# Kernel tuning notes

Hardware: AMD Instinct MI355X
Metric: run time of the kernel (lower is better)

## Reference

```python
import jax, jax.numpy as jnp
import numpy as np

E = 300000          # number of edges
C_IN = 128          # in_channels (source/target feature dim)
C_E = 128           # edge_channels
C_OUT = 128         # out_channels (== in_channels, required by AttentionBlock residual)
C8 = C_OUT // 8     # attention bottleneck dim


def _lin(key, fan_in, fan_out):
    # torch nn.Linear default: U(-1/sqrt(fan_in), 1/sqrt(fan_in)) for W and b
    kw, kb = jax.random.split(key)
    bound = 1.0 / np.sqrt(fan_in)
    w = jax.random.uniform(kw, (fan_in, fan_out), jnp.float32, -bound, bound)
    b = jax.random.uniform(kb, (fan_out,), jnp.float32, -bound, bound)
    return w, b


def setup_inputs() -> dict:
    key = jax.random.key(0)
    ks = jax.random.split(key, 10)
    w1, b1 = _lin(ks[3], 2 * C_IN + C_E, C_OUT)   # edge_mlp[0]
    w2, b2 = _lin(ks[4], C_OUT, C_OUT)            # edge_mlp[2]
    wg, bg = _lin(ks[5], C_OUT, C8)               # att.g
    wt, bt = _lin(ks[6], C_OUT, C8)               # att.theta
    wp, bp = _lin(ks[7], C_OUT, C8)               # att.phi
    wo, bo = _lin(ks[8], C8, C_OUT)               # att.W
    return {
        "source": jax.random.normal(ks[0], (E, C_IN), jnp.float32),
        "target": jax.random.normal(ks[1], (E, C_IN), jnp.float32),
        "edge_attr": jax.random.normal(ks[2], (E, C_E), jnp.float32),
        "w1": w1, "b1": b1, "w2": w2, "b2": b2,
        "wg": wg, "bg": bg, "wt": wt, "bt": bt,
        "wp": wp, "bp": bp, "wo": wo, "bo": bo,
    }


def reference(source, target, edge_attr, w1, b1, w2, b2, wg, bg, wt, bt, wp, bp, wo, bo):
    # edge_mlp: Linear -> ReLU -> Linear on concat(source, target, edge_attr)
    x = jnp.concatenate([source, target, edge_attr], axis=1)        # [E, 2*C_IN + C_E]
    h = jax.nn.relu(x @ w1 + b1)                                    # [E, C_OUT]
    h = h @ w2 + b2                                                 # [E, C_OUT]
    # AttentionBlock (AtLoc-style): rank-1 outer-product attention over bottleneck dim
    g = h @ wg + bg                                                 # [E, C8]
    th = h @ wt + bt                                                # [E, C8]
    ph = h @ wp + bp                                                # [E, C8]
    f = ph[:, :, None] * th[:, None, :]                             # [E, C8, C8] = phi_x @ theta_x^T
    a = jax.nn.softmax(f, axis=-1)                                  # softmax over last dim
    y = jnp.einsum("eij,ej->ei", a, g)                              # [E, C8]
    return y @ wo + bo + h                                          # residual add, [E, C_OUT]
```

## Files before the change

### kernel.cpp

```cpp
#include <hip/hip_runtime.h>
#include <hip/hip_bf16.h>

typedef unsigned short u16;
typedef unsigned int u32;
typedef __bf16 bf16x8 __attribute__((ext_vector_type(8)));
typedef float f32x4 __attribute__((ext_vector_type(4)));

#define NE 300000
#define NBLK 2344

#define WS_WT1   0
#define WS_WT2   49152
#define WS_WGTP  65536
#define WS_WO    71680
#define WS_TOTAL 75776
#define WS_BF32  37888
#define NBIAS    432
#define WS_FLAG32 38320

__device__ __forceinline__ float bs2f(u16 u) {
    union { u32 i; float f; } v; v.i = ((u32)u) << 16; return v.f;
}
__device__ __forceinline__ u16 f2bs(float f) {
    __hip_bfloat16 h = __float2bfloat16(f);
    u16 u; __builtin_memcpy(&u, &h, 2); return u;
}
__device__ __forceinline__ __bf16 f2b(float f) {
    __hip_bfloat16 h = __float2bfloat16(f);
    __bf16 b; __builtin_memcpy(&b, &h, 2); return b;
}

#define LDFRAG(arr, row, kch) (*(const bf16x8*)&(arr)[(row) * 128 + ((((kch) ^ ((row) & 15))) << 3)])
#define SWZ(row, col) ((row) * 128 + (((((col) >> 3) ^ ((row) & 15))) << 3) + ((col) & 7))

__global__ void sniff_kernel(const void* __restrict__ src, u32* __restrict__ wsu) {
    if (threadIdx.x != 0) return;
    const u32* p = (const u32*)src;
    int score = 0;
    for (int i = 0; i < 64; ++i) {
        u32 w = p[i];
        int e = (w >> 7) & 0xFF;
        score += (e > 100 && e < 150) ? 1 : 0;
    }
    wsu[WS_FLAG32] = (score >= 40) ? 1u : 0u;
}

__global__ void prep_kernel(const void* __restrict__ w1, const void* __restrict__ w2,
                            const void* __restrict__ wg, const void* __restrict__ wt,
                            const void* __restrict__ wp, const void* __restrict__ wo,
                            const void* __restrict__ b1, const void* __restrict__ b2,
                            const void* __restrict__ bg, const void* __restrict__ bt,
                            const void* __restrict__ bp, const void* __restrict__ bo,
                            u16* __restrict__ ws) {
    const bool isbf = ((const u32*)ws)[WS_FLAG32] != 0;
    auto ldf = [&](const void* p, int idx) -> float {
        return isbf ? bs2f(((const u16*)p)[idx]) : ((const float*)p)[idx];
    };
    int id = blockIdx.x * 256 + threadIdx.x;
    if (id < WS_TOTAL) {
        float v;
        if (id < WS_WT2) {
            int c = id >> 14, r = id & 16383, n = r >> 7, k = r & 127;
            v = ldf(w1, (c * 128 + k) * 128 + n);
        } else if (id < WS_WGTP) {
            int r = id - WS_WT2, n = r >> 7, k = r & 127;
            v = ldf(w2, k * 128 + n);
        } else if (id < WS_WO) {
            int r = id - WS_WGTP, n = r >> 7, k = r & 127;
            if (n < 16)      v = ldf(wg, k * 16 + n);
            else if (n < 32) v = ldf(wt, k * 16 + (n - 16));
            else             v = ldf(wp, k * 16 + (n - 32));
        } else {
            int r = id - WS_WO, n = r >> 5, k = r & 31;
            v = (k < 16) ? ldf(wo, k * 128 + n) : 0.f;
        }
        ws[id] = f2bs(v);
    } else if (id < WS_TOTAL + NBIAS) {
        int b = id - WS_TOTAL;
        float v;
        if (b < 128)      v = ldf(b1, b);
        else if (b < 256) v = ldf(b2, b - 128);
        else if (b < 272) v = ldf(bg, b - 256);
        else if (b < 288) v = ldf(bt, b - 272);
        else if (b < 304) v = ldf(bp, b - 288);
        else              v = ldf(bo, b - 304);
        ((float*)ws)[WS_BF32 + b] = v;
    }
}

#define GEMM_K128(NACC, ACC)                                                          \
    _Pragma("unroll")                                                                 \
    for (int kk = 0; kk < 4; ++kk) {                                                  \
        const int kch = kk * 4 + l4;                                                  \
        bf16x8 af0 = LDFRAG(lsA, 32 * w + l15, kch);                                  \
        bf16x8 af1 = LDFRAG(lsA, 32 * w + 16 + l15, kch);                             \
        _Pragma("unroll")                                                             \
        for (int c = 0; c < NACC; ++c) {                                              \
            bf16x8 bb = LDFRAG(lsB, 16 * c + l15, kch);                               \
            ACC[0][c] = __builtin_amdgcn_mfma_f32_16x16x32_bf16(af0, bb, ACC[0][c], 0, 0, 0); \
            ACC[1][c] = __builtin_amdgcn_mfma_f32_16x16x32_bf16(af1, bb, ACC[1][c], 0, 0, 0); \
        }                                                                             \
    }

__launch_bounds__(256, 2)
__global__ void fused_kernel(const void* __restrict__ gsrc, const void* __restrict__ gtgt,
                             const void* __restrict__ gea,
                             const u16* __restrict__ ws, void* __restrict__ gout) {
    __shared__ __align__(16) u16 ls[32768];
    u16* lsA = ls;
    u16* lsB = ls + 16384;

    const int t   = threadIdx.x;
    const int w   = t >> 6;
    const int l   = t & 63;
    const int l15 = l & 15;
    const int l4  = l >> 4;
    const long e0 = (long)blockIdx.x * 128;
    const bool isbf = ((const u32*)ws)[WS_FLAG32] != 0;
    const float* wsF = (const float*)ws + WS_BF32;

    f32x4 acc[2][8];
    f32x4 accp[2][3];

    #pragma unroll
    for (int r = 0; r < 2; ++r)
        #pragma unroll
        for (int c = 0; c < 8; ++c)
            acc[r][c] = (f32x4){0.f, 0.f, 0.f, 0.f};

    auto stageB = [&](const u16* __restrict__ g, int iters) {
        for (int i = 0; i < iters; ++i) {
            int o = i * 2048 + t * 8;
            int row = o >> 7, c = (o & 127) >> 3;
            uint4 v = *(const uint4*)(g + o);
            *(uint4*)&lsB[row * 128 + ((c ^ (row & 15)) << 3)] = v;
        }
    };

    #pragma unroll
    for (int kc = 0; kc < 3; ++kc) {
        const void* __restrict__ ga = (kc == 0) ? gsrc : (kc == 1) ? gtgt : gea;
        #pragma unroll
        for (int i = 0; i < 8; ++i) {
            int o = i * 2048 + t * 8;
            int row = o >> 7, col = o & 127;
            long ge = e0 + row; if (ge >= NE) ge = NE - 1;
            bf16x8 vb;
            if (isbf) {
                uint4 v = *(const uint4*)((const u16*)ga + ge * 128 + col);
                __builtin_memcpy(&vb, &v, 16);
            } else {
                const float* gf = (const float*)ga + ge * 128 + col;
                f32x4 a0 = *(const f32x4*)gf;
                f32x4 a1 = *(const f32x4*)(gf + 4);
                #pragma unroll
                for (int q = 0; q < 4; ++q) { vb[q] = f2b(a0[q]); vb[4 + q] = f2b(a1[q]); }
            }
            *(bf16x8*)&lsA[row * 128 + ((((col >> 3) ^ (row & 15))) << 3)] = vb;
        }
        stageB(ws + WS_WT1 + kc * 16384, 8);
        __syncthreads();
        GEMM_K128(8, acc)
        __syncthreads();
    }

    float bv[8];
    #pragma unroll
    for (int c = 0; c < 8; ++c) bv[c] = wsF[16 * c + l15];
    #pragma unroll
    for (int r = 0; r < 2; ++r)
        #pragma unroll
        for (int c = 0; c < 8; ++c)
            #pragma unroll
            for (int q = 0; q < 4; ++q) {
                float h = acc[r][c][q] + bv[c];
                h = h > 0.f ? h : 0.f;
                int row = 32 * w + 16 * r + 4 * l4 + q;
                int col = 16 * c + l15;
                lsA[SWZ(row, col)] = f2bs(h);
            }
    stageB(ws + WS_WT2, 8);
    __syncthreads();

    #pragma unroll
    for (int r = 0; r < 2; ++r)
        #pragma unroll
        for (int c = 0; c < 8; ++c)
            acc[r][c] = (f32x4){0.f, 0.f, 0.f, 0.f};
    GEMM_K128(8, acc)
    __syncthreads();

    #pragma unroll
    for (int c = 0; c < 8; ++c) bv[c] = wsF[128 + 16 * c + l15];
    #pragma unroll
    for (int r = 0; r < 2; ++r)
        #pragma unroll
        for (int c = 0; c < 8; ++c)
            #pragma unroll
            for (int q = 0; q < 4; ++q) {
                acc[r][c][q] += bv[c];
                int row = 32 * w + 16 * r + 4 * l4 + q;
                int col = 16 * c + l15;
                lsA[SWZ(row, col)] = f2bs(acc[r][c][q]);
            }
    stageB(ws + WS_WGTP, 3);
    __syncthreads();

    #pragma unroll
    for (int r = 0; r < 2; ++r)
        #pragma unroll
        for (int c = 0; c < 3; ++c)
            accp[r][c] = (f32x4){0.f, 0.f, 0.f, 0.f};
    GEMM_K128(3, accp)
    __syncthreads();

    float* projF = (float*)lsA;
    {
        float pb[3] = {wsF[256 + l15], wsF[272 + l15], wsF[288 + l15]};
        #pragma unroll
        for (int r = 0; r < 2; ++r)
            #pragma unroll
            for (int c = 0; c < 3; ++c)
                #pragma unroll
                for (int q = 0; q < 4; ++q) {
                    int row = 32 * w + 16 * r + 4 * l4 + q;
                    projF[row * 49 + 16 * c + l15] = accp[r][c][q] + pb[c];
                }
    }
    __syncthreads();

    {
        int er = t >> 1, hf = t & 1;
        const float* pr = projF + er * 49;
        float gg[16], tt[16];
        #pragma unroll
        for (int j = 0; j < 16; ++j) { gg[j] = pr[j]; tt[j] = pr[16 + j]; }
        float tmax = tt[0], tmin = tt[0];
        #pragma unroll
        for (int j = 1; j < 16; ++j) { tmax = fmaxf(tmax, tt[j]); tmin = fminf(tmin, tt[j]); }
        #pragma unroll
        for (int ii = 0; ii < 8; ++ii) {
            int iy = hf * 8 + ii;
            float s = pr[32 + iy];
            float m = (s >= 0.f) ? s * tmax : s * tmin;
            float den = 0.f, num = 0.f;
            #pragma unroll
            for (int j = 0; j < 16; ++j) {
                float e = __expf(fmaf(s, tt[j], -m));
                den += e;
                num = fmaf(e, gg[j], num);
            }
            float y = num / den;
            lsB[er * 32 + ((((iy >> 3) ^ (er & 3))) << 3) + (iy & 7)] = f2bs(y);
            int kz = iy + 16;
            lsB[er * 32 + ((((kz >> 3) ^ (er & 3))) << 3) + (kz & 7)] = 0;
        }
        #pragma unroll
        for (int s2 = 0; s2 < 2; ++s2) {
            int id = t * 16 + s2 * 8;
            int n = id >> 5, k = id & 31;
            uint4 v = *(const uint4*)(ws + WS_WO + id);
            *(uint4*)&lsB[4096 + n * 32 + ((((k >> 3) ^ (n & 3))) << 3)] = v;
        }
    }
    __syncthreads();

    {
        bf16x8 af0, af1, bq;
        {
            int m0 = 32 * w + l15;
            int m1 = 32 * w + 16 + l15;
            af0 = *(const bf16x8*)&lsB[m0 * 32 + (((l4 ^ (m0 & 3))) << 3)];
            af1 = *(const bf16x8*)&lsB[m1 * 32 + (((l4 ^ (m1 & 3))) << 3)];
        }
        #pragma unroll
        for (int c = 0; c < 8; ++c) {
            int n = 16 * c + l15;
            bq = *(const bf16x8*)&lsB[4096 + n * 32 + (((l4 ^ (n & 3))) << 3)];
            acc[0][c] = __builtin_amdgcn_mfma_f32_16x16x32_bf16(af0, bq, acc[0][c], 0, 0, 0);
            acc[1][c] = __builtin_amdgcn_mfma_f32_16x16x32_bf16(af1, bq, acc[1][c], 0, 0, 0);
        }
    }
    __syncthreads();

    #pragma unroll
    for (int c = 0; c < 8; ++c) bv[c] = wsF[304 + 16 * c + l15];

    if (!isbf) {
        float* lsF = (float*)ls;
        #pragma unroll
        for (int r = 0; r < 2; ++r)
            #pragma unroll
            for (int c = 0; c < 8; ++c)
                #pragma unroll
                for (int q = 0; q < 4; ++q) {
                    int row = 32 * w + 16 * r + 4 * l4 + q;
                    int col = 16 * c + l15;
                    lsF[row * 128 + col] = acc[r][c][q] + bv[c];
                }
        __syncthreads();
        float* gf = (float*)gout;
        #pragma unroll
        for (int i = 0; i < 16; ++i) {
            int o = i * 1024 + t * 4;
            int row = o >> 7, col = o & 127;
            long ge = e0 + row;
            if (ge < NE) *(uint4*)(gf + ge * 128 + col) = *(const uint4*)&lsF[o];
        }
    } else {
        #pragma unroll
        for (int r = 0; r < 2; ++r)
            #pragma unroll
            for (int c = 0; c < 8; ++c)
                #pragma unroll
                for (int q = 0; q < 4; ++q) {
                    int row = 32 * w + 16 * r + 4 * l4 + q;
                    int col = 16 * c + l15;
                    lsA[SWZ(row, col)] = f2bs(acc[r][c][q] + bv[c]);
                }
        __syncthreads();
        u16* gu = (u16*)gout;
        #pragma unroll
        for (int i = 0; i < 8; ++i) {
            int o = i * 2048 + t * 8;
            int row = o >> 7, col = o & 127;
            long ge = e0 + row;
            if (ge < NE) {
                uint4 v = *(const uint4*)&lsA[SWZ(row, col)];
                *(uint4*)(gu + ge * 128 + col) = v;
            }
        }
    }
}

extern "C" void kernel_launch(void* const* d_in, const int* in_sizes, int n_in,
                              void* d_out, int out_size, void* d_ws, size_t ws_size,
                              hipStream_t stream) {
    u16* ws = (u16*)d_ws;

    sniff_kernel<<<1, 64, 0, stream>>>(d_in[0], (u32*)d_ws);
    prep_kernel<<<(WS_TOTAL + NBIAS + 255) / 256, 256, 0, stream>>>(
        d_in[3], d_in[5], d_in[7], d_in[9], d_in[11], d_in[13],
        d_in[4], d_in[6], d_in[8], d_in[10], d_in[12], d_in[14], ws);
    fused_kernel<<<NBLK, 256, 0, stream>>>(d_in[0], d_in[1], d_in[2], ws, d_out);
}
```

Baseline: 521.9 us.

## Make each wave independent: direct global fragment loads, per-wave LDS, no block barriers

Each wave now owns 32 edge rows and a private 8 KB LDS slice. Activation fragments for the first GEMM are loaded straight from global memory into registers, and weight fragments for every GEMM are read directly from global/L2 instead of being staged into shared memory. This removes all __syncthreads and halves LDS use, so the launch bound rises to 4 blocks per CU. The trade-off is uncoalesced, repeated weight reads from L2 by every wave, and global loads that are no longer batched ahead of the MFMAs.

```diff
diff --git a/kernel.cpp b/kernel.cpp
--- a/kernel.cpp
+++ b/kernel.cpp
@@ -30,8 +30,8 @@
     __bf16 b; __builtin_memcpy(&b, &h, 2); return b;
 }
 
-#define LDFRAG(arr, row, kch) (*(const bf16x8*)&(arr)[(row) * 128 + ((((kch) ^ ((row) & 15))) << 3)])
-#define SWZ(row, col) ((row) * 128 + (((((col) >> 3) ^ ((row) & 15))) << 3) + ((col) & 7))
+#define LDFRAG(base, lr, kch) (*(const bf16x8*)&(base)[(lr) * 128 + ((((kch) ^ ((lr) & 15))) << 3)])
+#define SWZ(lr, col) ((lr) * 128 + (((((col) >> 3) ^ ((lr) & 15))) << 3) + ((col) & 7))
 
 __global__ void sniff_kernel(const void* __restrict__ src, u32* __restrict__ wsu) {
     if (threadIdx.x != 0) return;
@@ -88,80 +88,79 @@
     }
 }
 
-#define GEMM_K128(NACC, ACC)                                                          \
+#define GEMM_K128_L2(NACC, ACC, BP)                                                   \
     _Pragma("unroll")                                                                 \
     for (int kk = 0; kk < 4; ++kk) {                                                  \
         const int kch = kk * 4 + l4;                                                  \
-        bf16x8 af0 = LDFRAG(lsA, 32 * w + l15, kch);                                  \
-        bf16x8 af1 = LDFRAG(lsA, 32 * w + 16 + l15, kch);                             \
+        bf16x8 af0 = LDFRAG(mls, l15, kch);                                           \
+        bf16x8 af1 = LDFRAG(mls, 16 + l15, kch);                                      \
         _Pragma("unroll")                                                             \
         for (int c = 0; c < NACC; ++c) {                                              \
-            bf16x8 bb = LDFRAG(lsB, 16 * c + l15, kch);                               \
+            uint4 bw = *(const uint4*)((BP) + (16 * c + l15) * 128 + kch * 8);        \
+            bf16x8 bb; __builtin_memcpy(&bb, &bw, 16);                                \
             ACC[0][c] = __builtin_amdgcn_mfma_f32_16x16x32_bf16(af0, bb, ACC[0][c], 0, 0, 0); \
             ACC[1][c] = __builtin_amdgcn_mfma_f32_16x16x32_bf16(af1, bb, ACC[1][c], 0, 0, 0); \
         }                                                                             \
     }
 
-__launch_bounds__(256, 2)
+__launch_bounds__(256, 4)
 __global__ void fused_kernel(const void* __restrict__ gsrc, const void* __restrict__ gtgt,
                              const void* __restrict__ gea,
                              const u16* __restrict__ ws, void* __restrict__ gout) {
-    __shared__ __align__(16) u16 ls[32768];
-    u16* lsA = ls;
-    u16* lsB = ls + 16384;
+    __shared__ __align__(16) u16 ls[16384];
 
     const int t   = threadIdx.x;
     const int w   = t >> 6;
     const int l   = t & 63;
     const int l15 = l & 15;
     const int l4  = l >> 4;
-    const long e0 = (long)blockIdx.x * 128;
+    u16* mls = ls + (w << 12);
+    const long e0 = (long)blockIdx.x * 128 + 32 * w;
     const bool isbf = ((const u32*)ws)[WS_FLAG32] != 0;
     const float* wsF = (const float*)ws + WS_BF32;
 
+    long geA = e0 + l15;      if (geA >= NE) geA = NE - 1;
+    long geB = e0 + 16 + l15; if (geB >= NE) geB = NE - 1;
+
     f32x4 acc[2][8];
-    f32x4 accp[2][3];
-
     #pragma unroll
     for (int r = 0; r < 2; ++r)
         #pragma unroll
         for (int c = 0; c < 8; ++c)
             acc[r][c] = (f32x4){0.f, 0.f, 0.f, 0.f};
 
-    auto stageB = [&](const u16* __restrict__ g, int iters) {
-        for (int i = 0; i < iters; ++i) {
-            int o = i * 2048 + t * 8;
-            int row = o >> 7, c = (o & 127) >> 3;
-            uint4 v = *(const uint4*)(g + o);
-            *(uint4*)&lsB[row * 128 + ((c ^ (row & 15)) << 3)] = v;
-        }
-    };
-
     #pragma unroll
     for (int kc = 0; kc < 3; ++kc) {
         const void* __restrict__ ga = (kc == 0) ? gsrc : (kc == 1) ? gtgt : gea;
-        #pragma unroll
-        for (int i = 0; i < 8; ++i) {
-            int o = i * 2048 + t * 8;
-            int row = o >> 7, col = o & 127;
-            long ge = e0 + row; if (ge >= NE) ge = NE - 1;
-            bf16x8 vb;
+        const u16* bp = ws + WS_WT1 + kc * 16384;
+        #pragma unroll
+        for (int kk = 0; kk < 4; ++kk) {
+            const int kch = kk * 4 + l4;
+            bf16x8 af0, af1;
             if (isbf) {
-                uint4 v = *(const uint4*)((const u16*)ga + ge * 128 + col);
-                __builtin_memcpy(&vb, &v, 16);
+                uint4 v0 = *(const uint4*)((const u16*)ga + geA * 128 + kch * 8);
+                uint4 v1 = *(const uint4*)((const u16*)ga + geB * 128 + kch * 8);
+                __builtin_memcpy(&af0, &v0, 16);
+                __builtin_memcpy(&af1, &v1, 16);
             } else {
-                const float* gf = (const float*)ga + ge * 128 + col;
-                f32x4 a0 = *(const f32x4*)gf;
-                f32x4 a1 = *(const f32x4*)(gf + 4);
+                const float* f0 = (const float*)ga + geA * 128 + kch * 8;
+                const float* f1 = (const float*)ga + geB * 128 + kch * 8;
+                f32x4 a0 = *(const f32x4*)f0, a1 = *(const f32x4*)(f0 + 4);
+                f32x4 c0 = *(const f32x4*)f1, c1 = *(const f32x4*)(f1 + 4);
                 #pragma unroll
-                for (int q = 0; q < 4; ++q) { vb[q] = f2b(a0[q]); vb[4 + q] = f2b(a1[q]); }
-            }
-            *(bf16x8*)&lsA[row * 128 + ((((col >> 3) ^ (row & 15))) << 3)] = vb;
-        }
-        stageB(ws + WS_WT1 + kc * 16384, 8);
-        __syncthreads();
-        GEMM_K128(8, acc)
-        __syncthreads();
+                for (int q = 0; q < 4; ++q) {
+                    af0[q] = f2b(a0[q]); af0[4 + q] = f2b(a1[q]);
+                    af1[q] = f2b(c0[q]); af1[4 + q] = f2b(c1[q]);
+                }
+            }
+            #pragma unroll
+            for (int c = 0; c < 8; ++c) {
+                uint4 bw = *(const uint4*)(bp + (16 * c + l15) * 128 + kch * 8);
+                bf16x8 bb; __builtin_memcpy(&bb, &bw, 16);
+                acc[0][c] = __builtin_amdgcn_mfma_f32_16x16x32_bf16(af0, bb, acc[0][c], 0, 0, 0);
+                acc[1][c] = __builtin_amdgcn_mfma_f32_16x16x32_bf16(af1, bb, acc[1][c], 0, 0, 0);
+            }
+        }
     }
 
     float bv[8];
@@ -175,20 +174,17 @@
             for (int q = 0; q < 4; ++q) {
                 float h = acc[r][c][q] + bv[c];
                 h = h > 0.f ? h : 0.f;
-                int row = 32 * w + 16 * r + 4 * l4 + q;
+                int lr = 16 * r + 4 * l4 + q;
                 int col = 16 * c + l15;
-                lsA[SWZ(row, col)] = f2bs(h);
-            }
-    stageB(ws + WS_WT2, 8);
-    __syncthreads();
+                mls[SWZ(lr, col)] = f2bs(h);
+            }
 
     #pragma unroll
     for (int r = 0; r < 2; ++r)
         #pragma unroll
         for (int c = 0; c < 8; ++c)
             acc[r][c] = (f32x4){0.f, 0.f, 0.f, 0.f};
-    GEMM_K128(8, acc)
-    __syncthreads();
+    GEMM_K128_L2(8, acc, ws + WS_WT2)
 
     #pragma unroll
     for (int c = 0; c < 8; ++c) bv[c] = wsF[128 + 16 * c + l15];
@@ -199,22 +195,20 @@
             #pragma unroll
             for (int q = 0; q < 4; ++q) {
                 acc[r][c][q] += bv[c];
-                int row = 32 * w + 16 * r + 4 * l4 + q;
+                int lr = 16 * r + 4 * l4 + q;
                 int col = 16 * c + l15;
-                lsA[SWZ(row, col)] = f2bs(acc[r][c][q]);
-            }
-    stageB(ws + WS_WGTP, 3);
-    __syncthreads();
-
+                mls[SWZ(lr, col)] = f2bs(acc[r][c][q]);
+            }
+
+    f32x4 accp[2][3];
     #pragma unroll
     for (int r = 0; r < 2; ++r)
         #pragma unroll
         for (int c = 0; c < 3; ++c)
             accp[r][c] = (f32x4){0.f, 0.f, 0.f, 0.f};
-    GEMM_K128(3, accp)
-    __syncthreads();
-
-    float* projF = (float*)lsA;
+    GEMM_K128_L2(3, accp, ws + WS_WGTP)
+
+    float* projF = (float*)mls;
     {
         float pb[3] = {wsF[256 + l15], wsF[272 + l15], wsF[288 + l15]};
         #pragma unroll
@@ -223,25 +217,26 @@
             for (int c = 0; c < 3; ++c)
                 #pragma unroll
                 for (int q = 0; q < 4; ++q) {
-                    int row = 32 * w + 16 * r + 4 * l4 + q;
-                    projF[row * 49 + 16 * c + l15] = accp[r][c][q] + pb[c];
+                    int lr = 16 * r + 4 * l4 + q;
+                    projF[lr * 49 + 16 * c + l15] = accp[r][c][q] + pb[c];
                 }
     }
-    __syncthreads();
 
     {
-        int er = t >> 1, hf = t & 1;
+        int er = l >> 1, hf = l & 1;
         const float* pr = projF + er * 49;
-        float gg[16], tt[16];
+        float gg[16], tt[16], ss[8];
         #pragma unroll
         for (int j = 0; j < 16; ++j) { gg[j] = pr[j]; tt[j] = pr[16 + j]; }
+        #pragma unroll
+        for (int ii = 0; ii < 8; ++ii) ss[ii] = pr[32 + hf * 8 + ii];
         float tmax = tt[0], tmin = tt[0];
         #pragma unroll
         for (int j = 1; j < 16; ++j) { tmax = fmaxf(tmax, tt[j]); tmin = fminf(tmin, tt[j]); }
+        bf16x8 yv;
         #pragma unroll
         for (int ii = 0; ii < 8; ++ii) {
-            int iy = hf * 8 + ii;
-            float s = pr[32 + iy];
+            float s = ss[ii];
             float m = (s >= 0.f) ? s * tmax : s * tmin;
             float den = 0.f, num = 0.f;
             #pragma unroll
@@ -250,83 +245,69 @@
                 den += e;
                 num = fmaf(e, gg[j], num);
             }
-            float y = num / den;
-            lsB[er * 32 + ((((iy >> 3) ^ (er & 3))) << 3) + (iy & 7)] = f2bs(y);
-            int kz = iy + 16;
-            lsB[er * 32 + ((((kz >> 3) ^ (er & 3))) << 3) + (kz & 7)] = 0;
-        }
-        #pragma unroll
-        for (int s2 = 0; s2 < 2; ++s2) {
-            int id = t * 16 + s2 * 8;
-            int n = id >> 5, k = id & 31;
-            uint4 v = *(const uint4*)(ws + WS_WO + id);
-            *(uint4*)&lsB[4096 + n * 32 + ((((k >> 3) ^ (n & 3))) << 3)] = v;
-        }
-    }
-    __syncthreads();
+            yv[ii] = f2b(num / den);
+        }
+        u16* yb = mls + 3072;
+        *(bf16x8*)&yb[er * 32 + ((hf ^ (er & 3)) << 3)] = yv;
+        bf16x8 zv; __builtin_memset(&zv, 0, 16);
+        *(bf16x8*)&yb[er * 32 + (((2 + hf) ^ (er & 3)) << 3)] = zv;
+    }
 
     {
-        bf16x8 af0, af1, bq;
-        {
-            int m0 = 32 * w + l15;
-            int m1 = 32 * w + 16 + l15;
-            af0 = *(const bf16x8*)&lsB[m0 * 32 + (((l4 ^ (m0 & 3))) << 3)];
-            af1 = *(const bf16x8*)&lsB[m1 * 32 + (((l4 ^ (m1 & 3))) << 3)];
-        }
+        const u16* yb = mls + 3072;
+        int m0 = l15, m1 = 16 + l15;
+        bf16x8 af0 = *(const bf16x8*)&yb[m0 * 32 + ((l4 ^ (m0 & 3)) << 3)];
+        bf16x8 af1 = *(const bf16x8*)&yb[m1 * 32 + ((l4 ^ (m1 & 3)) << 3)];
         #pragma unroll
         for (int c = 0; c < 8; ++c) {
             int n = 16 * c + l15;
-            bq = *(const bf16x8*)&lsB[4096 + n * 32 + (((l4 ^ (n & 3))) << 3)];
+            uint4 bw = *(const uint4*)(ws + WS_WO + n * 32 + l4 * 8);
+            bf16x8 bq; __builtin_memcpy(&bq, &bw, 16);
             acc[0][c] = __builtin_amdgcn_mfma_f32_16x16x32_bf16(af0, bq, acc[0][c], 0, 0, 0);
             acc[1][c] = __builtin_amdgcn_mfma_f32_16x16x32_bf16(af1, bq, acc[1][c], 0, 0, 0);
         }
     }
-    __syncthreads();
 
     #pragma unroll
     for (int c = 0; c < 8; ++c) bv[c] = wsF[304 + 16 * c + l15];
 
     if (!isbf) {
-        float* lsF = (float*)ls;
+        float* lsF = (float*)mls;
+        float* gf = (float*)gout;
+        #pragma unroll
+        for (int r = 0; r < 2; ++r) {
+            #pragma unroll
+            for (int c = 0; c < 8; ++c)
+                #pragma unroll
+                for (int q = 0; q < 4; ++q)
+                    lsF[(4 * l4 + q) * 128 + 16 * c + l15] = acc[r][c][q] + bv[c];
+            #pragma unroll
+            for (int i = 0; i < 8; ++i) {
+                int idx = i * 256 + l * 4;
+                int lr = idx >> 7, col = idx & 127;
+                long ge = e0 + 16 * r + lr;
+                if (ge < NE) *(uint4*)(gf + ge * 128 + col) = *(const uint4*)&lsF[idx];
+            }
+        }
+    } else {
         #pragma unroll
         for (int r = 0; r < 2; ++r)
             #pragma unroll
             for (int c = 0; c < 8; ++c)
                 #pragma unroll
                 for (int q = 0; q < 4; ++q) {
-                    int row = 32 * w + 16 * r + 4 * l4 + q;
+                    int lr = 16 * r + 4 * l4 + q;
                     int col = 16 * c + l15;
-                    lsF[row * 128 + col] = acc[r][c][q] + bv[c];
+                    mls[SWZ(lr, col)] = f2bs(acc[r][c][q] + bv[c]);
                 }
-        __syncthreads();
-        float* gf = (float*)gout;
-        #pragma unroll
-        for (int i = 0; i < 16; ++i) {
-            int o = i * 1024 + t * 4;
-            int row = o >> 7, col = o & 127;
-            long ge = e0 + row;
-            if (ge < NE) *(uint4*)(gf + ge * 128 + col) = *(const uint4*)&lsF[o];
-        }
-    } else {
-        #pragma unroll
-        for (int r = 0; r < 2; ++r)
-            #pragma unroll
-            for (int c = 0; c < 8; ++c)
-                #pragma unroll
-                for (int q = 0; q < 4; ++q) {
-                    int row = 32 * w + 16 * r + 4 * l4 + q;
-                    int col = 16 * c + l15;
-                    lsA[SWZ(row, col)] = f2bs(acc[r][c][q] + bv[c]);
-                }
-        __syncthreads();
         u16* gu = (u16*)gout;
         #pragma unroll
         for (int i = 0; i < 8; ++i) {
-            int o = i * 2048 + t * 8;
-            int row = o >> 7, col = o & 127;
-            long ge = e0 + row;
+            int idx = i * 512 + l * 8;
+            int lr = idx >> 7, col = idx & 127;
+            long ge = e0 + lr;
             if (ge < NE) {
-                uint4 v = *(const uint4*)&lsA[SWZ(row, col)];
+                uint4 v = *(const uint4*)&mls[SWZ(lr, col)];
                 *(uint4*)(gu + ge * 128 + col) = v;
             }
         }
```

Measured after the change: 755.9 us. 44.8% more time.
